# Kernel optimization log

Hardware: AMD Instinct MI355X
Metric: run time of the kernel (lower is better)

The kernel has to match this reference:

```python
import jax, jax.numpy as jnp
import numpy as np

VOCAB = 32000
EMBED = 512
HIDDEN = 1024
PAD_IDX = 0


def setup_inputs() -> dict:
    key = jax.random.key(0)
    ks = jax.random.split(key, 6)
    input_tokens = jax.random.randint(ks[0], (16, 256), 0, VOCAB, dtype=jnp.int32)
    emb = jax.random.normal(ks[1], (VOCAB, EMBED), dtype=jnp.float32)
    Wxh = jax.random.normal(ks[2], (EMBED, HIDDEN), dtype=jnp.float32) * (1.0 / np.sqrt(EMBED))
    Whh = jax.random.normal(ks[3], (HIDDEN, HIDDEN), dtype=jnp.float32) * (1.0 / np.sqrt(HIDDEN))
    bias = jnp.zeros((HIDDEN,), dtype=jnp.float32)
    # nn.Linear(hidden, vocab) init: uniform(-1/sqrt(hidden), 1/sqrt(hidden))
    bound = 1.0 / np.sqrt(HIDDEN)
    Wout = jax.random.uniform(ks[4], (HIDDEN, VOCAB), dtype=jnp.float32, minval=-bound, maxval=bound)
    bout = jax.random.uniform(ks[5], (VOCAB,), dtype=jnp.float32, minval=-bound, maxval=bound)
    return {"input_tokens": input_tokens, "emb": emb, "Wxh": Wxh, "Whh": Whh,
            "bias": bias, "Wout": Wout, "bout": bout}


def reference(input_tokens, emb, Wxh, Whh, bias, Wout, bout):
    # padding_idx row is zero (as in nn.Embedding(padding_idx=...))
    emb = emb.at[PAD_IDX].set(0.0)
    x = emb[input_tokens]                      # [B, T, E]
    B = x.shape[0]
    # precompute input projections for all steps (linear, order-independent)
    xproj = jnp.einsum('bte,eh->bth', x, Wxh) + bias  # [B, T, H]
    h0 = jnp.zeros((B, HIDDEN), dtype=x.dtype)

    def step(h, xp_t):
        h_new = jnp.tanh(xp_t + h @ Whh)
        return h_new, h_new

    _, hs = jax.lax.scan(step, h0, jnp.swapaxes(xproj, 0, 1))  # hs: [T, B, H]
    hs = jnp.swapaxes(hs, 0, 1)                                # [B, T, H]
    logits = jnp.einsum('bth,hv->btv', hs, Wout) + bout        # [B, T, V]
    return logits
```

## Files before the change

kernel.cpp:

```cpp
#include <hip/hip_runtime.h>
#include <math.h>

#define VOCAB  32000
#define EMBED  512
#define HIDDEN 1024
#define BATCH  16
#define SEQ    256
#define M_TOTAL (BATCH*SEQ)
#define RNN_BLOCKS 64
#define COLS 16
#define NFLAGS ((SEQ-1)*RNN_BLOCKS)
#define RSTRIDE 1028

typedef __attribute__((ext_vector_type(8))) short short8;
typedef __attribute__((ext_vector_type(4))) float f32x4;

static __device__ __forceinline__ unsigned short f2bf(float x) {
    unsigned int u = __float_as_uint(x);
    unsigned int r = (u + 0x7FFFu + ((u >> 16) & 1u)) >> 16;
    return (unsigned short)r;
}
static __device__ __forceinline__ float bf2f(unsigned short b) {
    return __uint_as_float(((unsigned int)b) << 16);
}

__global__ __launch_bounds__(256) void k_zero(int* __restrict__ flags) {
    const int i = blockIdx.x * 256 + threadIdx.x;
    if (i < NFLAGS) flags[i] = 0;
}

__global__ __launch_bounds__(256) void k_embed_xproj(
    const int* __restrict__ tok, const float* __restrict__ emb,
    const float* __restrict__ Wxh, const float* __restrict__ bias,
    float* __restrict__ xproj)
{
    __shared__ float At[16][68];
    __shared__ float Bt[16][68];
    const int row0 = blockIdx.y * 64;
    const int col0 = blockIdx.x * 64;
    const int tid = threadIdx.x;
    const int tx = tid & 15, ty = tid >> 4;

    const int am = tid >> 2, aq = tid & 3;
    const int bn = tid & 15, bk = tid >> 4;

    const int tokid = tok[row0 + am];
    const float4* embrow = (tokid == 0) ? (const float4*)nullptr
                         : (const float4*)(emb + (size_t)tokid * EMBED);

    float acc[4][4] = {};

    for (int k0 = 0; k0 < EMBED; k0 += 16) {
        float4 av = make_float4(0.f, 0.f, 0.f, 0.f);
        if (embrow) av = embrow[(k0 >> 2) + aq];
        float4 bv = *(const float4*)(Wxh + (size_t)(k0 + bk) * HIDDEN + col0 + bn * 4);

        __syncthreads();
        At[aq*4+0][am] = av.x; At[aq*4+1][am] = av.y;
        At[aq*4+2][am] = av.z; At[aq*4+3][am] = av.w;
        *(float4*)&Bt[bk][bn*4] = bv;
        __syncthreads();

        #pragma unroll
        for (int k = 0; k < 16; ++k) {
            float4 a = *(const float4*)&At[k][ty*4];
            float4 b = *(const float4*)&Bt[k][tx*4];
            float aa[4] = {a.x, a.y, a.z, a.w};
            float bb[4] = {b.x, b.y, b.z, b.w};
            #pragma unroll
            for (int i = 0; i < 4; ++i)
                #pragma unroll
                for (int j = 0; j < 4; ++j)
                    acc[i][j] = fmaf(aa[i], bb[j], acc[i][j]);
        }
    }

    float4 bb = *(const float4*)(bias + col0 + tx*4);
    #pragma unroll
    for (int i = 0; i < 4; ++i) {
        const int row = row0 + ty*4 + i;
        float4 v = make_float4(acc[i][0] + bb.x, acc[i][1] + bb.y,
                               acc[i][2] + bb.z, acc[i][3] + bb.w);
        *(float4*)(xproj + (size_t)row * HIDDEN + col0 + tx*4) = v;
    }
}

__global__ __launch_bounds__(256) void k_rnn(
    const float* __restrict__ xproj, const float* __restrict__ Whh,
    float* __restrict__ hs, int* __restrict__ flags)
{
    __shared__ float wl[COLS * RSTRIDE];
    __shared__ float hl[BATCH * RSTRIDE];
    const int bid = blockIdx.x;
    const int tid = threadIdx.x;
    const int ks  = tid & 15;
    const int bc  = tid >> 4;
    const int b4  = bc >> 2;
    const int c4  = bc & 3;
    const int lane = tid & 63;

    {
        const int c = tid & 15, kk = tid >> 4;
        for (int i = 0; i < 64; ++i) {
            const int k = kk + (i << 4);
            const float v = Whh[(size_t)k * HIDDEN + bid * COLS + c];
            const int s = k >> 2, e = k & 3;
            const int sw = s ^ ((s >> 4) & 15);
            wl[c * RSTRIDE + sw * 4 + e] = v;
        }
    }
    __syncthreads();

    const int ob = b4 * 4 + (ks >> 2);
    const int oc = c4 * 4 + (ks & 3);
    const int cg = bid * COLS + oc;

    for (int t = 0; t < SEQ; ++t) {
        const float xp = xproj[((size_t)ob * SEQ + t) * HIDDEN + cg];
        float acc[4][4] = {};
        if (t > 0) {
            f32x4 tmp[BATCH];
            #pragma unroll
            for (int bb = 0; bb < BATCH; ++bb) {
                const float* p = hs + ((size_t)bb * SEQ + (t - 1)) * HIDDEN + tid * 4;
                asm volatile("global_load_dwordx4 %0, %1, off sc0 sc1"
                             : "=&v"(tmp[bb]) : "v"(p));
            }
            asm volatile("s_waitcnt vmcnt(0)" ::: "memory");
            const int swf = (tid ^ ((tid >> 4) & 15)) * 4;
            #pragma unroll
            for (int bb = 0; bb < BATCH; ++bb)
                *(f32x4*)&hl[bb * RSTRIDE + swf] = tmp[bb];
            __syncthreads();
            const int ks16 = ks * 16;
            #pragma unroll 4
            for (int kq = 0; kq < 16; ++kq) {
                const int sp = ((ks16 + kq) ^ ks) * 4;
                float4 h4[4], w4[4];
                #pragma unroll
                for (int i = 0; i < 4; ++i)
                    h4[i] = *(const float4*)&hl[(b4*4 + i) * RSTRIDE + sp];
                #pragma unroll
                for (int j = 0; j < 4; ++j)
                    w4[j] = *(const float4*)&wl[(c4*4 + j) * RSTRIDE + sp];
                #pragma unroll
                for (int i = 0; i < 4; ++i)
                    #pragma unroll
                    for (int j = 0; j < 4; ++j) {
                        acc[i][j] = fmaf(h4[i].x, w4[j].x, acc[i][j]);
                        acc[i][j] = fmaf(h4[i].y, w4[j].y, acc[i][j]);
                        acc[i][j] = fmaf(h4[i].z, w4[j].z, acc[i][j]);
                        acc[i][j] = fmaf(h4[i].w, w4[j].w, acc[i][j]);
                    }
            }
        }
        #pragma unroll
        for (int off = 8; off >= 1; off >>= 1)
            #pragma unroll
            for (int i = 0; i < 4; ++i)
                #pragma unroll
                for (int j = 0; j < 4; ++j)
                    acc[i][j] += __shfl_xor(acc[i][j], off, 16);

        const float val = tanhf(xp + acc[ks >> 2][ks & 3]);
        __hip_atomic_store(hs + ((size_t)ob * SEQ + t) * HIDDEN + cg, val,
                           __ATOMIC_RELAXED, __HIP_MEMORY_SCOPE_SYSTEM);

        if (t < SEQ - 1) {
            asm volatile("s_waitcnt vmcnt(0)" ::: "memory");
            __syncthreads();
            if (tid == 0)
                __hip_atomic_store(&flags[t * RNN_BLOCKS + bid], 1,
                                   __ATOMIC_RELAXED, __HIP_MEMORY_SCOPE_SYSTEM);
            while (__hip_atomic_load(&flags[t * RNN_BLOCKS + lane],
                                     __ATOMIC_RELAXED, __HIP_MEMORY_SCOPE_SYSTEM) == 0)
                __builtin_amdgcn_s_sleep(1);
            __syncthreads();
        }
    }
}

__global__ __launch_bounds__(256) void k_cvt_hs(
    const float* __restrict__ src, unsigned short* __restrict__ h,
    unsigned short* __restrict__ l)
{
    const size_t i = ((size_t)blockIdx.x * 256 + threadIdx.x) * 4;
    const float4 v = *(const float4*)(src + i);
    float f[4] = {v.x, v.y, v.z, v.w};
    unsigned short hh[4], ll[4];
    #pragma unroll
    for (int e = 0; e < 4; ++e) {
        hh[e] = f2bf(f[e]);
        ll[e] = f2bf(f[e] - bf2f(hh[e]));
    }
    *(ushort4*)(h + i) = make_ushort4(hh[0], hh[1], hh[2], hh[3]);
    *(ushort4*)(l + i) = make_ushort4(ll[0], ll[1], ll[2], ll[3]);
}

__global__ __launch_bounds__(256) void k_cvt_wT(
    const float* __restrict__ W, unsigned short* __restrict__ WTh,
    unsigned short* __restrict__ WTl)
{
    __shared__ float t[64][68];
    const int n0 = blockIdx.x * 64, k0 = blockIdx.y * 64;
    const int tid = threadIdx.x;
    const int r = tid >> 4, c4 = tid & 15;
    #pragma unroll
    for (int p = 0; p < 4; ++p) {
        const float4 v = *(const float4*)(W + (size_t)(k0 + r + p*16) * VOCAB + n0 + c4*4);
        *(float4*)&t[r + p*16][c4*4] = v;
    }
    __syncthreads();
    #pragma unroll
    for (int p = 0; p < 4; ++p) {
        const int rn = r + p * 16;
        unsigned short hh[4], ll[4];
        #pragma unroll
        for (int j = 0; j < 4; ++j) {
            const float x = t[c4*4 + j][rn];
            hh[j] = f2bf(x);
            ll[j] = f2bf(x - bf2f(hh[j]));
        }
        const size_t o = (size_t)(n0 + rn) * HIDDEN + k0 + c4*4;
        *(ushort4*)(WTh + o) = make_ushort4(hh[0], hh[1], hh[2], hh[3]);
        *(ushort4*)(WTl + o) = make_ushort4(ll[0], ll[1], ll[2], ll[3]);
    }
}

__global__ __launch_bounds__(256) void k_logits_mfma(
    const unsigned short* __restrict__ Ahp, const unsigned short* __restrict__ Alp,
    const unsigned short* __restrict__ Bhp, const unsigned short* __restrict__ Blp,
    const float* __restrict__ bout, float* __restrict__ out)
{
    __shared__ unsigned short sAh[128*32], sAl[128*32], sBh[128*32], sBl[128*32];
    const int bid0 = blockIdx.x;
    const int sid = (bid0 & 7) * (8000 / 8) + (bid0 >> 3);
    const int n0 = (sid >> 5) * 128;
    const int m0 = (sid & 31) * 128;
    const int tid = threadIdx.x;
    const int wv = tid >> 6, l = tid & 63;
    const int wr = wv >> 1, wc = wv & 1;
    const int rr = l & 15, kb = l >> 4;

    f32x4 acc[4][4];
    #pragma unroll
    for (int i = 0; i < 4; ++i)
        #pragma unroll
        for (int j = 0; j < 4; ++j) acc[i][j] = (f32x4)0.f;

    const int sr = tid >> 2, q = tid & 3;

    for (int kt = 0; kt < 32; ++kt) {
        const int k0 = kt * 32;
        __syncthreads();
        #pragma unroll
        for (int p = 0; p < 2; ++p) {
            const int r = sr + p * 64;
            const int ws = (q ^ ((r >> 1) & 3)) << 3;
            const size_t ga = (size_t)(m0 + r) * HIDDEN + k0 + q * 8;
            const size_t gb = (size_t)(n0 + r) * HIDDEN + k0 + q * 8;
            *(short8*)&sAh[r*32 + ws] = *(const short8*)(Ahp + ga);
            *(short8*)&sAl[r*32 + ws] = *(const short8*)(Alp + ga);
            *(short8*)&sBh[r*32 + ws] = *(const short8*)(Bhp + gb);
            *(short8*)&sBl[r*32 + ws] = *(const short8*)(Blp + gb);
        }
        __syncthreads();

        short8 fah[4], fal[4], fbh[4], fbl[4];
        #pragma unroll
        for (int i = 0; i < 4; ++i) {
            const int ra = wr*64 + i*16 + rr;
            const int sa = ra*32 + ((kb ^ ((ra >> 1) & 3)) << 3);
            fah[i] = *(const short8*)&sAh[sa];
            fal[i] = *(const short8*)&sAl[sa];
            const int rb = wc*64 + i*16 + rr;
            const int sb = rb*32 + ((kb ^ ((rb >> 1) & 3)) << 3);
            fbh[i] = *(const short8*)&sBh[sb];
            fbl[i] = *(const short8*)&sBl[sb];
        }
        #pragma unroll
        for (int i = 0; i < 4; ++i)
            #pragma unroll
            for (int j = 0; j < 4; ++j) {
                acc[i][j] = __builtin_amdgcn_mfma_f32_16x16x32_bf16(fah[i], fbh[j], acc[i][j], 0, 0, 0);
                acc[i][j] = __builtin_amdgcn_mfma_f32_16x16x32_bf16(fah[i], fbl[j], acc[i][j], 0, 0, 0);
                acc[i][j] = __builtin_amdgcn_mfma_f32_16x16x32_bf16(fal[i], fbh[j], acc[i][j], 0, 0, 0);
            }
    }

    #pragma unroll
    for (int j = 0; j < 4; ++j) {
        const int col = n0 + wc*64 + j*16 + rr;
        const float bj = bout[col];
        #pragma unroll
        for (int i = 0; i < 4; ++i) {
            const int row0 = m0 + wr*64 + i*16 + kb*4;
            #pragma unroll
            for (int p = 0; p < 4; ++p)
                out[(size_t)(row0 + p) * VOCAB + col] = acc[i][j][p] + bj;
        }
    }
}

__global__ __launch_bounds__(256) void k_logits(
    const float* __restrict__ hs, const float* __restrict__ Wout,
    const float* __restrict__ bout, float* __restrict__ out)
{
    __shared__ float At[16][132];
    __shared__ float Bt[16][132];
    const int col0 = blockIdx.x * 128;
    const int row0 = blockIdx.y * 128;
    const int tid = threadIdx.x;
    const int tx = tid & 15, ty = tid >> 4;

    float acc[8][8] = {};

    for (int k0 = 0; k0 < HIDDEN; k0 += 16) {
        float4 av[2], bv[2];
        #pragma unroll
        for (int p = 0; p < 2; ++p) {
            const int idx = tid + p * 256;
            const int m = idx >> 2, qq = idx & 3;
            av[p] = *(const float4*)(hs + (size_t)(row0 + m) * HIDDEN + k0 + qq * 4);
            const int n4 = idx & 31, kk = idx >> 5;
            bv[p] = *(const float4*)(Wout + (size_t)(k0 + kk) * VOCAB + col0 + n4 * 4);
        }
        __syncthreads();
        #pragma unroll
        for (int p = 0; p < 2; ++p) {
            const int idx = tid + p * 256;
            const int m = idx >> 2, qq = idx & 3;
            At[qq*4+0][m] = av[p].x; At[qq*4+1][m] = av[p].y;
            At[qq*4+2][m] = av[p].z; At[qq*4+3][m] = av[p].w;
            const int n4 = idx & 31, kk = idx >> 5;
            *(float4*)&Bt[kk][n4*4] = bv[p];
        }
        __syncthreads();

        #pragma unroll
        for (int k = 0; k < 16; ++k) {
            float a[8], b[8];
            *(float4*)&a[0] = *(const float4*)&At[k][ty*4];
            *(float4*)&a[4] = *(const float4*)&At[k][64 + ty*4];
            *(float4*)&b[0] = *(const float4*)&Bt[k][tx*4];
            *(float4*)&b[4] = *(const float4*)&Bt[k][64 + tx*4];
            #pragma unroll
            for (int i = 0; i < 8; ++i)
                #pragma unroll
                for (int j = 0; j < 8; ++j)
                    acc[i][j] = fmaf(a[i], b[j], acc[i][j]);
        }
    }

    const float4 blo = *(const float4*)(bout + col0 + tx*4);
    const float4 bhi = *(const float4*)(bout + col0 + 64 + tx*4);
    #pragma unroll
    for (int ih = 0; ih < 2; ++ih)
        #pragma unroll
        for (int i = 0; i < 4; ++i) {
            const int row = row0 + ih*64 + ty*4 + i;
            float* orow = out + (size_t)row * VOCAB + col0;
            const int r = ih*4 + i;
            float4 v0 = make_float4(acc[r][0] + blo.x, acc[r][1] + blo.y,
                                    acc[r][2] + blo.z, acc[r][3] + blo.w);
            float4 v1 = make_float4(acc[r][4] + bhi.x, acc[r][5] + bhi.y,
                                    acc[r][6] + bhi.z, acc[r][7] + bhi.w);
            *(float4*)(orow + tx*4) = v0;
            *(float4*)(orow + 64 + tx*4) = v1;
        }
}

extern "C" void kernel_launch(void* const* d_in, const int* in_sizes, int n_in,
                              void* d_out, int out_size, void* d_ws, size_t ws_size,
                              hipStream_t stream) {
    const int*   tok  = (const int*)d_in[0];
    const float* emb  = (const float*)d_in[1];
    const float* Wxh  = (const float*)d_in[2];
    const float* Whh  = (const float*)d_in[3];
    const float* bias = (const float*)d_in[4];
    const float* Wout = (const float*)d_in[5];
    const float* bout = (const float*)d_in[6];
    float* out = (float*)d_out;

    char* ws = (char*)d_ws;
    int* flags = (int*)ws;

    const size_t OFF_HS   = 65536;
    const size_t OFF_HSH  = OFF_HS  + (size_t)M_TOTAL * HIDDEN * 4;
    const size_t OFF_HSL  = OFF_HSH + (size_t)M_TOTAL * HIDDEN * 2;
    const size_t OFF_WTH  = OFF_HSL + (size_t)M_TOTAL * HIDDEN * 2;
    const size_t OFF_WTL  = OFF_WTH + (size_t)VOCAB * HIDDEN * 2;
    const size_t OFF_XP   = OFF_WTL + (size_t)VOCAB * HIDDEN * 2;
    const size_t NEED     = OFF_XP  + (size_t)M_TOTAL * HIDDEN * 4;

    if (ws_size >= NEED) {
        float*          hs   = (float*)(ws + OFF_HS);
        unsigned short* hsh  = (unsigned short*)(ws + OFF_HSH);
        unsigned short* hsl  = (unsigned short*)(ws + OFF_HSL);
        unsigned short* wth  = (unsigned short*)(ws + OFF_WTH);
        unsigned short* wtl  = (unsigned short*)(ws + OFF_WTL);
        float*          xproj= (float*)(ws + OFF_XP);

        hipLaunchKernelGGL(k_zero, dim3(64), dim3(256), 0, stream, flags);
        hipLaunchKernelGGL(k_embed_xproj, dim3(HIDDEN/64, M_TOTAL/64), dim3(256), 0, stream,
                           tok, emb, Wxh, bias, xproj);
        hipLaunchKernelGGL(k_rnn, dim3(RNN_BLOCKS), dim3(256), 0, stream,
                           xproj, Whh, hs, flags);
        hipLaunchKernelGGL(k_cvt_hs, dim3(M_TOTAL*HIDDEN/1024), dim3(256), 0, stream,
                           hs, hsh, hsl);
        hipLaunchKernelGGL(k_cvt_wT, dim3(VOCAB/64, HIDDEN/64), dim3(256), 0, stream,
                           Wout, wth, wtl);
        hipLaunchKernelGGL(k_logits_mfma, dim3((VOCAB/128)*(M_TOTAL/128)), dim3(256), 0, stream,
                           hsh, hsl, wth, wtl, bout, out);
    } else {
        float* xproj = (float*)(ws + 65536);
        float* hs    = (float*)(ws + 65536 + (size_t)M_TOTAL * HIDDEN * 4);

        hipLaunchKernelGGL(k_zero, dim3(64), dim3(256), 0, stream, flags);
        hipLaunchKernelGGL(k_embed_xproj, dim3(HIDDEN/64, M_TOTAL/64), dim3(256), 0, stream,
                           tok, emb, Wxh, bias, xproj);
        hipLaunchKernelGGL(k_rnn, dim3(RNN_BLOCKS), dim3(256), 0, stream,
                           xproj, Whh, hs, flags);
        hipLaunchKernelGGL(k_logits, dim3(VOCAB/128, M_TOTAL/128), dim3(256), 0, stream,
                           hs, Wout, bout, out);
    }
}
```

Baseline: 3.150 ms.

## Keep recurrent weight slice in registers and widen RNN blocks to 512 threads

The recurrent kernel now loads each block's Whh column slice once into per-thread registers (32 float4s) instead of rereading it from LDS every step, which frees shared memory for the hidden-state tile. It moves to 512 threads per block, splitting the K reduction across 32 lanes, and prefetches the next step's xproj value. The inter-block flag handshake changes from relaxed system scope to release/acquire agent scope. The intent is to cut LDS traffic and per-step latency in the serial recurrence, at the cost of heavy register pressure (launch_bounds 512,2), a longer shuffle reduction, and an extra barrier per step.

```diff
diff --git a/kernel.cpp b/kernel.cpp
--- a/kernel.cpp
+++ b/kernel.cpp
@@ -85,95 +85,126 @@
     }
 }
 
-__global__ __launch_bounds__(256) void k_rnn(
+__global__ __launch_bounds__(512, 2) void k_rnn(
     const float* __restrict__ xproj, const float* __restrict__ Whh,
     float* __restrict__ hs, int* __restrict__ flags)
 {
-    __shared__ float wl[COLS * RSTRIDE];
-    __shared__ float hl[BATCH * RSTRIDE];
+    __shared__ float smem[COLS * RSTRIDE];
     const int bid = blockIdx.x;
     const int tid = threadIdx.x;
-    const int ks  = tid & 15;
-    const int bc  = tid >> 4;
-    const int b4  = bc >> 2;
-    const int c4  = bc & 3;
+    const int ks  = tid & 31;
+    const int c4  = (tid >> 5) & 3;
+    const int b4  = tid >> 7;
     const int lane = tid & 63;
 
     {
         const int c = tid & 15, kk = tid >> 4;
-        for (int i = 0; i < 64; ++i) {
-            const int k = kk + (i << 4);
-            const float v = Whh[(size_t)k * HIDDEN + bid * COLS + c];
-            const int s = k >> 2, e = k & 3;
-            const int sw = s ^ ((s >> 4) & 15);
-            wl[c * RSTRIDE + sw * 4 + e] = v;
+        for (int i = 0; i < 32; ++i) {
+            const int k = kk + (i << 5);
+            smem[c * RSTRIDE + k] = Whh[(size_t)k * HIDDEN + bid * COLS + c];
         }
     }
     __syncthreads();
 
-    const int ob = b4 * 4 + (ks >> 2);
-    const int oc = c4 * 4 + (ks & 3);
-    const int cg = bid * COLS + oc;
+    f32x4 wreg[32];
+    #pragma unroll
+    for (int kk2 = 0; kk2 < 32; ++kk2) {
+        const int kidx = ks * 32 + kk2;
+        f32x4 w;
+        #pragma unroll
+        for (int j = 0; j < 4; ++j)
+            w[j] = smem[(c4 * 4 + j) * RSTRIDE + kidx];
+        wreg[kk2] = w;
+    }
+    __syncthreads();
+
+    const int myb  = b4 * 4 + ((ks & 15) >> 2);
+    const int myc  = c4 * 4 + (ks & 3);
+    const int mycg = bid * COLS + myc;
+    const bool wr  = (ks < 16);
+
+    float xp_pref = xproj[((size_t)myb * SEQ + 0) * HIDDEN + mycg];
 
     for (int t = 0; t < SEQ; ++t) {
-        const float xp = xproj[((size_t)ob * SEQ + t) * HIDDEN + cg];
-        float acc[4][4] = {};
+        const float xp = xp_pref;
+        if (t + 1 < SEQ)
+            xp_pref = xproj[((size_t)myb * SEQ + (t + 1)) * HIDDEN + mycg];
+
+        f32x4 acc0 = (f32x4)0.f, acc1 = (f32x4)0.f,
+              acc2 = (f32x4)0.f, acc3 = (f32x4)0.f;
+
         if (t > 0) {
-            f32x4 tmp[BATCH];
-            #pragma unroll
-            for (int bb = 0; bb < BATCH; ++bb) {
-                const float* p = hs + ((size_t)bb * SEQ + (t - 1)) * HIDDEN + tid * 4;
+            f32x4 tmp[8];
+            #pragma unroll
+            for (int p = 0; p < 8; ++p) {
+                const int g = p * 512 + tid;
+                const int b = g >> 8, s = g & 255;
+                const float* ptr = hs + ((size_t)b * SEQ + (t - 1)) * HIDDEN + s * 4;
                 asm volatile("global_load_dwordx4 %0, %1, off sc0 sc1"
-                             : "=&v"(tmp[bb]) : "v"(p));
+                             : "=&v"(tmp[p]) : "v"(ptr));
             }
             asm volatile("s_waitcnt vmcnt(0)" ::: "memory");
-            const int swf = (tid ^ ((tid >> 4) & 15)) * 4;
-            #pragma unroll
-            for (int bb = 0; bb < BATCH; ++bb)
-                *(f32x4*)&hl[bb * RSTRIDE + swf] = tmp[bb];
+            #pragma unroll
+            for (int p = 0; p < 8; ++p) {
+                const int g = p * 512 + tid;
+                const int b = g >> 8, s = g & 255;
+                const int ss = (s & ~7) | ((s & 7) ^ ((s >> 3) & 7));
+                *(f32x4*)&smem[b * RSTRIDE + ss * 4] = tmp[p];
+            }
             __syncthreads();
-            const int ks16 = ks * 16;
-            #pragma unroll 4
-            for (int kq = 0; kq < 16; ++kq) {
-                const int sp = ((ks16 + kq) ^ ks) * 4;
-                float4 h4[4], w4[4];
+
+            #pragma unroll
+            for (int kq = 0; kq < 8; ++kq) {
+                const int sp = (ks * 8 + (kq ^ (ks & 7))) * 4;
+                const f32x4 h0 = *(const f32x4*)&smem[(b4*4+0) * RSTRIDE + sp];
+                const f32x4 h1 = *(const f32x4*)&smem[(b4*4+1) * RSTRIDE + sp];
+                const f32x4 h2 = *(const f32x4*)&smem[(b4*4+2) * RSTRIDE + sp];
+                const f32x4 h3 = *(const f32x4*)&smem[(b4*4+3) * RSTRIDE + sp];
                 #pragma unroll
-                for (int i = 0; i < 4; ++i)
-                    h4[i] = *(const float4*)&hl[(b4*4 + i) * RSTRIDE + sp];
-                #pragma unroll
-                for (int j = 0; j < 4; ++j)
-                    w4[j] = *(const float4*)&wl[(c4*4 + j) * RSTRIDE + sp];
-                #pragma unroll
-                for (int i = 0; i < 4; ++i)
-                    #pragma unroll
-                    for (int j = 0; j < 4; ++j) {
-                        acc[i][j] = fmaf(h4[i].x, w4[j].x, acc[i][j]);
-                        acc[i][j] = fmaf(h4[i].y, w4[j].y, acc[i][j]);
-                        acc[i][j] = fmaf(h4[i].z, w4[j].z, acc[i][j]);
-                        acc[i][j] = fmaf(h4[i].w, w4[j].w, acc[i][j]);
-                    }
-            }
-        }
-        #pragma unroll
-        for (int off = 8; off >= 1; off >>= 1)
-            #pragma unroll
-            for (int i = 0; i < 4; ++i)
-                #pragma unroll
-                for (int j = 0; j < 4; ++j)
-                    acc[i][j] += __shfl_xor(acc[i][j], off, 16);
-
-        const float val = tanhf(xp + acc[ks >> 2][ks & 3]);
-        __hip_atomic_store(hs + ((size_t)ob * SEQ + t) * HIDDEN + cg, val,
-                           __ATOMIC_RELAXED, __HIP_MEMORY_SCOPE_SYSTEM);
+                for (int e = 0; e < 4; ++e) {
+                    const f32x4 w = wreg[kq * 4 + e];
+                    acc0 += h0[e] * w;
+                    acc1 += h1[e] * w;
+                    acc2 += h2[e] * w;
+                    acc3 += h3[e] * w;
+                }
+            }
+            __syncthreads();
+        }
+
+        #pragma unroll
+        for (int off = 16; off >= 1; off >>= 1) {
+            #pragma unroll
+            for (int e = 0; e < 4; ++e) {
+                acc0[e] += __shfl_xor(acc0[e], off, 32);
+                acc1[e] += __shfl_xor(acc1[e], off, 32);
+                acc2[e] += __shfl_xor(acc2[e], off, 32);
+                acc3[e] += __shfl_xor(acc3[e], off, 32);
+            }
+        }
+
+        if (wr) {
+            float val = 0.f;
+            #pragma unroll
+            for (int j = 0; j < 4; ++j) {
+                if (ks == 0*4 + j) val = acc0[j];
+                if (ks == 1*4 + j) val = acc1[j];
+                if (ks == 2*4 + j) val = acc2[j];
+                if (ks == 3*4 + j) val = acc3[j];
+            }
+            const float res = tanhf(xp + val);
+            __hip_atomic_store(hs + ((size_t)myb * SEQ + t) * HIDDEN + mycg, res,
+                               __ATOMIC_RELAXED, __HIP_MEMORY_SCOPE_SYSTEM);
+        }
 
         if (t < SEQ - 1) {
             asm volatile("s_waitcnt vmcnt(0)" ::: "memory");
             __syncthreads();
             if (tid == 0)
                 __hip_atomic_store(&flags[t * RNN_BLOCKS + bid], 1,
-                                   __ATOMIC_RELAXED, __HIP_MEMORY_SCOPE_SYSTEM);
+                                   __ATOMIC_RELEASE, __HIP_MEMORY_SCOPE_AGENT);
             while (__hip_atomic_load(&flags[t * RNN_BLOCKS + lane],
-                                     __ATOMIC_RELAXED, __HIP_MEMORY_SCOPE_SYSTEM) == 0)
+                                     __ATOMIC_ACQUIRE, __HIP_MEMORY_SCOPE_AGENT) == 0)
                 __builtin_amdgcn_s_sleep(1);
             __syncthreads();
         }
@@ -404,7 +435,7 @@
         hipLaunchKernelGGL(k_zero, dim3(64), dim3(256), 0, stream, flags);
         hipLaunchKernelGGL(k_embed_xproj, dim3(HIDDEN/64, M_TOTAL/64), dim3(256), 0, stream,
                            tok, emb, Wxh, bias, xproj);
-        hipLaunchKernelGGL(k_rnn, dim3(RNN_BLOCKS), dim3(256), 0, stream,
+        hipLaunchKernelGGL(k_rnn, dim3(RNN_BLOCKS), dim3(512), 0, stream,
                            xproj, Whh, hs, flags);
         hipLaunchKernelGGL(k_cvt_hs, dim3(M_TOTAL*HIDDEN/1024), dim3(256), 0, stream,
                            hs, hsh, hsl);
@@ -419,7 +450,7 @@
         hipLaunchKernelGGL(k_zero, dim3(64), dim3(256), 0, stream, flags);
         hipLaunchKernelGGL(k_embed_xproj, dim3(HIDDEN/64, M_TOTAL/64), dim3(256), 0, stream,
                            tok, emb, Wxh, bias, xproj);
-        hipLaunchKernelGGL(k_rnn, dim3(RNN_BLOCKS), dim3(256), 0, stream,
+        hipLaunchKernelGGL(k_rnn, dim3(RNN_BLOCKS), dim3(512), 0, stream,
                            xproj, Whh, hs, flags);
         hipLaunchKernelGGL(k_logits, dim3(VOCAB/128, M_TOTAL/128), dim3(256), 0, stream,
                            hs, Wout, bout, out);
```

Measured after the change: 5.181 ms. 64.5% more time.

## Keep Whh slice in registers, prefetch xproj, reuse LDS, relax flag scope

Applied to the files above, without the earlier changes.

Each thread now loads its Whh weights once into a 64-entry float4 register array instead of re-reading them from shared memory every timestep. One shared buffer is then reused for the hidden-state staging, and the next step's xproj value is prefetched. The inter-block flags switch from relaxed system-scope to release/acquire agent-scope atomics, and the spin sleep grows. This cuts LDS traffic and sync latency on the serial recurrence, at the cost of 256 extra VGPRs per thread and a longer polling interval that may add wakeup latency.

```diff
diff --git a/kernel.cpp b/kernel.cpp
--- a/kernel.cpp
+++ b/kernel.cpp
@@ -85,12 +85,11 @@
     }
 }
 
-__global__ __launch_bounds__(256) void k_rnn(
+__global__ __launch_bounds__(256, 1) void k_rnn(
     const float* __restrict__ xproj, const float* __restrict__ Whh,
     float* __restrict__ hs, int* __restrict__ flags)
 {
-    __shared__ float wl[COLS * RSTRIDE];
-    __shared__ float hl[BATCH * RSTRIDE];
+    __shared__ float smem[COLS * RSTRIDE];
     const int bid = blockIdx.x;
     const int tid = threadIdx.x;
     const int ks  = tid & 15;
@@ -106,17 +105,33 @@
             const float v = Whh[(size_t)k * HIDDEN + bid * COLS + c];
             const int s = k >> 2, e = k & 3;
             const int sw = s ^ ((s >> 4) & 15);
-            wl[c * RSTRIDE + sw * 4 + e] = v;
-        }
-    }
+            smem[c * RSTRIDE + sw * 4 + e] = v;
+        }
+    }
+    __syncthreads();
+
+    const int ks16 = ks * 16;
+    f32x4 wreg[4][16];
+    #pragma unroll
+    for (int j = 0; j < 4; ++j)
+        #pragma unroll
+        for (int kq = 0; kq < 16; ++kq) {
+            const int sp = ((ks16 + kq) ^ ks) * 4;
+            wreg[j][kq] = *(const f32x4*)&smem[(c4 * 4 + j) * RSTRIDE + sp];
+        }
     __syncthreads();
 
     const int ob = b4 * 4 + (ks >> 2);
     const int oc = c4 * 4 + (ks & 3);
     const int cg = bid * COLS + oc;
 
+    float xp_pref = xproj[((size_t)ob * SEQ + 0) * HIDDEN + cg];
+
     for (int t = 0; t < SEQ; ++t) {
-        const float xp = xproj[((size_t)ob * SEQ + t) * HIDDEN + cg];
+        const float xp = xp_pref;
+        if (t + 1 < SEQ)
+            xp_pref = xproj[((size_t)ob * SEQ + (t + 1)) * HIDDEN + cg];
+
         float acc[4][4] = {};
         if (t > 0) {
             f32x4 tmp[BATCH];
@@ -130,27 +145,25 @@
             const int swf = (tid ^ ((tid >> 4) & 15)) * 4;
             #pragma unroll
             for (int bb = 0; bb < BATCH; ++bb)
-                *(f32x4*)&hl[bb * RSTRIDE + swf] = tmp[bb];
+                *(f32x4*)&smem[bb * RSTRIDE + swf] = tmp[bb];
             __syncthreads();
-            const int ks16 = ks * 16;
-            #pragma unroll 4
+
+            #pragma unroll
             for (int kq = 0; kq < 16; ++kq) {
                 const int sp = ((ks16 + kq) ^ ks) * 4;
-                float4 h4[4], w4[4];
+                float4 h4[4];
                 #pragma unroll
                 for (int i = 0; i < 4; ++i)
-                    h4[i] = *(const float4*)&hl[(b4*4 + i) * RSTRIDE + sp];
-                #pragma unroll
-                for (int j = 0; j < 4; ++j)
-                    w4[j] = *(const float4*)&wl[(c4*4 + j) * RSTRIDE + sp];
+                    h4[i] = *(const float4*)&smem[(b4*4 + i) * RSTRIDE + sp];
                 #pragma unroll
                 for (int i = 0; i < 4; ++i)
                     #pragma unroll
                     for (int j = 0; j < 4; ++j) {
-                        acc[i][j] = fmaf(h4[i].x, w4[j].x, acc[i][j]);
-                        acc[i][j] = fmaf(h4[i].y, w4[j].y, acc[i][j]);
-                        acc[i][j] = fmaf(h4[i].z, w4[j].z, acc[i][j]);
-                        acc[i][j] = fmaf(h4[i].w, w4[j].w, acc[i][j]);
+                        const f32x4 w = wreg[j][kq];
+                        acc[i][j] = fmaf(h4[i].x, w[0], acc[i][j]);
+                        acc[i][j] = fmaf(h4[i].y, w[1], acc[i][j]);
+                        acc[i][j] = fmaf(h4[i].z, w[2], acc[i][j]);
+                        acc[i][j] = fmaf(h4[i].w, w[3], acc[i][j]);
                     }
             }
         }
@@ -171,10 +184,10 @@
             __syncthreads();
             if (tid == 0)
                 __hip_atomic_store(&flags[t * RNN_BLOCKS + bid], 1,
-                                   __ATOMIC_RELAXED, __HIP_MEMORY_SCOPE_SYSTEM);
+                                   __ATOMIC_RELEASE, __HIP_MEMORY_SCOPE_AGENT);
             while (__hip_atomic_load(&flags[t * RNN_BLOCKS + lane],
-                                     __ATOMIC_RELAXED, __HIP_MEMORY_SCOPE_SYSTEM) == 0)
-                __builtin_amdgcn_s_sleep(1);
+                                     __ATOMIC_ACQUIRE, __HIP_MEMORY_SCOPE_AGENT) == 0)
+                __builtin_amdgcn_s_sleep(4);
             __syncthreads();
         }
     }
```

Measured after the change: 5.700 ms. 1.81x slower.

## Overlap Wout conversion with RNN recurrence and fuse hs bf16 split into RNN

Applied to the files above, without the earlier changes.

Adds 192 extra blocks to the RNN launch that transpose and split Wout into bf16 hi/lo parts while the 64 recurrence blocks run on otherwise idle compute units. The RNN blocks also write the bf16 hi/lo split of each hidden state directly, which removes the separate hs conversion kernel and its extra pass over hs. The risk is that the converter blocks compete with the latency-bound recurrence for memory bandwidth and L2. Correctness also depends on all 64 recurrence blocks being co-resident with the converter blocks, since the spin-wait flags need them all running.

```diff
diff --git a/kernel.cpp b/kernel.cpp
--- a/kernel.cpp
+++ b/kernel.cpp
@@ -8,6 +8,7 @@
 #define SEQ    256
 #define M_TOTAL (BATCH*SEQ)
 #define RNN_BLOCKS 64
+#define CONVBLKS 192
 #define COLS 16
 #define NFLAGS ((SEQ-1)*RNN_BLOCKS)
 #define RSTRIDE 1028
@@ -87,12 +88,49 @@
 
 __global__ __launch_bounds__(256) void k_rnn(
     const float* __restrict__ xproj, const float* __restrict__ Whh,
-    float* __restrict__ hs, int* __restrict__ flags)
+    float* __restrict__ hs, int* __restrict__ flags,
+    unsigned short* __restrict__ hsh, unsigned short* __restrict__ hsl,
+    const float* __restrict__ Wout,
+    unsigned short* __restrict__ wth, unsigned short* __restrict__ wtl)
 {
     __shared__ float wl[COLS * RSTRIDE];
     __shared__ float hl[BATCH * RSTRIDE];
     const int bid = blockIdx.x;
     const int tid = threadIdx.x;
+
+    if (bid >= RNN_BLOCKS) {
+        const int cb = bid - RNN_BLOCKS;
+        float (*tt)[68] = (float(*)[68])wl;
+        const int r = tid >> 4, cc = tid & 15;
+        for (int p = cb; p < (VOCAB/64) * (HIDDEN/64); p += CONVBLKS) {
+            const int n0 = (p % (VOCAB/64)) * 64;
+            const int k0 = (p / (VOCAB/64)) * 64;
+            #pragma unroll
+            for (int q = 0; q < 4; ++q) {
+                const float4 v = *(const float4*)(Wout +
+                    (size_t)(k0 + r + q*16) * VOCAB + n0 + cc*4);
+                *(float4*)&tt[r + q*16][cc*4] = v;
+            }
+            __syncthreads();
+            #pragma unroll
+            for (int q = 0; q < 4; ++q) {
+                const int rn = r + q * 16;
+                unsigned short hh4[4], ll4[4];
+                #pragma unroll
+                for (int j = 0; j < 4; ++j) {
+                    const float x = tt[cc*4 + j][rn];
+                    hh4[j] = f2bf(x);
+                    ll4[j] = f2bf(x - bf2f(hh4[j]));
+                }
+                const size_t o = (size_t)(n0 + rn) * HIDDEN + k0 + cc*4;
+                *(ushort4*)(wth + o) = make_ushort4(hh4[0], hh4[1], hh4[2], hh4[3]);
+                *(ushort4*)(wtl + o) = make_ushort4(ll4[0], ll4[1], ll4[2], ll4[3]);
+            }
+            __syncthreads();
+        }
+        return;
+    }
+
     const int ks  = tid & 15;
     const int bc  = tid >> 4;
     const int b4  = bc >> 2;
@@ -117,6 +155,7 @@
 
     for (int t = 0; t < SEQ; ++t) {
         const float xp = xproj[((size_t)ob * SEQ + t) * HIDDEN + cg];
+
         float acc[4][4] = {};
         if (t > 0) {
             f32x4 tmp[BATCH];
@@ -163,8 +202,14 @@
                     acc[i][j] += __shfl_xor(acc[i][j], off, 16);
 
         const float val = tanhf(xp + acc[ks >> 2][ks & 3]);
-        __hip_atomic_store(hs + ((size_t)ob * SEQ + t) * HIDDEN + cg, val,
+        const size_t orow = ((size_t)ob * SEQ + t) * HIDDEN + cg;
+        __hip_atomic_store(hs + orow, val,
                            __ATOMIC_RELAXED, __HIP_MEMORY_SCOPE_SYSTEM);
+        if (hsh) {
+            const unsigned short hi = f2bf(val);
+            hsh[orow] = hi;
+            hsl[orow] = f2bf(val - bf2f(hi));
+        }
 
         if (t < SEQ - 1) {
             asm volatile("s_waitcnt vmcnt(0)" ::: "memory");
@@ -177,53 +222,6 @@
                 __builtin_amdgcn_s_sleep(1);
             __syncthreads();
         }
-    }
-}
-
-__global__ __launch_bounds__(256) void k_cvt_hs(
-    const float* __restrict__ src, unsigned short* __restrict__ h,
-    unsigned short* __restrict__ l)
-{
-    const size_t i = ((size_t)blockIdx.x * 256 + threadIdx.x) * 4;
-    const float4 v = *(const float4*)(src + i);
-    float f[4] = {v.x, v.y, v.z, v.w};
-    unsigned short hh[4], ll[4];
-    #pragma unroll
-    for (int e = 0; e < 4; ++e) {
-        hh[e] = f2bf(f[e]);
-        ll[e] = f2bf(f[e] - bf2f(hh[e]));
-    }
-    *(ushort4*)(h + i) = make_ushort4(hh[0], hh[1], hh[2], hh[3]);
-    *(ushort4*)(l + i) = make_ushort4(ll[0], ll[1], ll[2], ll[3]);
-}
-
-__global__ __launch_bounds__(256) void k_cvt_wT(
-    const float* __restrict__ W, unsigned short* __restrict__ WTh,
-    unsigned short* __restrict__ WTl)
-{
-    __shared__ float t[64][68];
-    const int n0 = blockIdx.x * 64, k0 = blockIdx.y * 64;
-    const int tid = threadIdx.x;
-    const int r = tid >> 4, c4 = tid & 15;
-    #pragma unroll
-    for (int p = 0; p < 4; ++p) {
-        const float4 v = *(const float4*)(W + (size_t)(k0 + r + p*16) * VOCAB + n0 + c4*4);
-        *(float4*)&t[r + p*16][c4*4] = v;
-    }
-    __syncthreads();
-    #pragma unroll
-    for (int p = 0; p < 4; ++p) {
-        const int rn = r + p * 16;
-        unsigned short hh[4], ll[4];
-        #pragma unroll
-        for (int j = 0; j < 4; ++j) {
-            const float x = t[c4*4 + j][rn];
-            hh[j] = f2bf(x);
-            ll[j] = f2bf(x - bf2f(hh[j]));
-        }
-        const size_t o = (size_t)(n0 + rn) * HIDDEN + k0 + c4*4;
-        *(ushort4*)(WTh + o) = make_ushort4(hh[0], hh[1], hh[2], hh[3]);
-        *(ushort4*)(WTl + o) = make_ushort4(ll[0], ll[1], ll[2], ll[3]);
     }
 }
 
@@ -404,12 +402,8 @@
         hipLaunchKernelGGL(k_zero, dim3(64), dim3(256), 0, stream, flags);
         hipLaunchKernelGGL(k_embed_xproj, dim3(HIDDEN/64, M_TOTAL/64), dim3(256), 0, stream,
                            tok, emb, Wxh, bias, xproj);
-        hipLaunchKernelGGL(k_rnn, dim3(RNN_BLOCKS), dim3(256), 0, stream,
-                           xproj, Whh, hs, flags);
-        hipLaunchKernelGGL(k_cvt_hs, dim3(M_TOTAL*HIDDEN/1024), dim3(256), 0, stream,
-                           hs, hsh, hsl);
-        hipLaunchKernelGGL(k_cvt_wT, dim3(VOCAB/64, HIDDEN/64), dim3(256), 0, stream,
-                           Wout, wth, wtl);
+        hipLaunchKernelGGL(k_rnn, dim3(RNN_BLOCKS + CONVBLKS), dim3(256), 0, stream,
+                           xproj, Whh, hs, flags, hsh, hsl, Wout, wth, wtl);
         hipLaunchKernelGGL(k_logits_mfma, dim3((VOCAB/128)*(M_TOTAL/128)), dim3(256), 0, stream,
                            hsh, hsl, wth, wtl, bout, out);
     } else {
@@ -420,7 +414,10 @@
         hipLaunchKernelGGL(k_embed_xproj, dim3(HIDDEN/64, M_TOTAL/64), dim3(256), 0, stream,
                            tok, emb, Wxh, bias, xproj);
         hipLaunchKernelGGL(k_rnn, dim3(RNN_BLOCKS), dim3(256), 0, stream,
-                           xproj, Whh, hs, flags);
+                           xproj, Whh, hs, flags,
+                           (unsigned short*)nullptr, (unsigned short*)nullptr,
+                           (const float*)nullptr,
+                           (unsigned short*)nullptr, (unsigned short*)nullptr);
         hipLaunchKernelGGL(k_logits, dim3(VOCAB/128, M_TOTAL/128), dim3(256), 0, stream,
                            hs, Wout, bout, out);
     }
```

New measurement: 3.085 ms. 2.1% less time.
